# Kernel tuning notes

Measured on AMD Instinct MI355X. Metric: run time of the kernel, lower is better.

Reference implementation:

```python
import jax, jax.numpy as jnp
import numpy as np
import math

NUM_HEADS = 16
SIZE = 1024
HEAD_SIZE = SIZE // NUM_HEADS
B, S = 2, 2048


def setup_inputs() -> dict:
    key = jax.random.key(0)
    ks = jax.random.split(key, 11)
    sc = 1.0 / math.sqrt(SIZE)
    inp = {
        "q": jax.random.normal(ks[0], (B, S, SIZE), dtype=jnp.float32),
        "k": jax.random.normal(ks[1], (B, S, SIZE), dtype=jnp.float32),
        "v": jax.random.normal(ks[2], (B, S, SIZE), dtype=jnp.float32),
        "Wq": jax.random.normal(ks[3], (SIZE, SIZE), dtype=jnp.float32) * sc,
        "bq": jax.random.normal(ks[4], (SIZE,), dtype=jnp.float32) * sc,
        "Wk": jax.random.normal(ks[5], (SIZE, SIZE), dtype=jnp.float32) * sc,
        "bk": jax.random.normal(ks[6], (SIZE,), dtype=jnp.float32) * sc,
        "Wv": jax.random.normal(ks[7], (SIZE, SIZE), dtype=jnp.float32) * sc,
        "bv": jax.random.normal(ks[8], (SIZE,), dtype=jnp.float32) * sc,
        "Wo": jax.random.normal(ks[9], (SIZE, SIZE), dtype=jnp.float32) * sc,
        "bo": jax.random.normal(ks[10], (SIZE,), dtype=jnp.float32) * sc,
    }
    return inp


def _split_heads(x):
    # [B, S, SIZE] -> [B, H, S, D]
    b, s, _ = x.shape
    return x.reshape(b, s, NUM_HEADS, HEAD_SIZE).transpose(0, 2, 1, 3)


def reference(q, k, v, Wq, bq, Wk, bk, Wv, bv, Wo, bo):
    qh = _split_heads(q @ Wq.T + bq) / math.sqrt(HEAD_SIZE)  # [B,H,S,D]
    kh = _split_heads(k @ Wk.T + bk)
    vh = _split_heads(v @ Wv.T + bv)
    scores = jnp.einsum("bhqd,bhkd->bhqk", qh, kh)  # [B,H,S,S]
    attn = jax.nn.softmax(scores, axis=-1)
    ctx = jnp.einsum("bhqk,bhkd->bhqd", attn, vh)  # [B,H,S,D]
    ctx = ctx.transpose(0, 2, 1, 3).reshape(q.shape[0], -1, SIZE)
    return ctx @ Wo.T + bo
```

## Files before the change

kernel.cpp:

```cpp
#include <hip/hip_runtime.h>
#include <hip/hip_bf16.h>

#define SIZE 1024
#define NH 16
#define HD 64
#define BB 2
#define SS 2048
#define MROWS (BB * SS)

using bf16 = __hip_bfloat16;
using frag16 = __attribute__((ext_vector_type(8))) short;
using f32x4 = __attribute__((ext_vector_type(4))) float;
typedef unsigned int u32;

__device__ __forceinline__ void glds16(const bf16* g, bf16* l) {
    __builtin_amdgcn_global_load_lds(
        (const __attribute__((address_space(1))) u32*)g,
        (__attribute__((address_space(3))) u32*)l, 16, 0, 0);
}

__device__ __forceinline__ void cvt_store8(bf16* dst, const float* src) {
    float4 a = *(const float4*)src;
    float4 b = *(const float4*)(src + 4);
    bf16 t[8];
    t[0] = __float2bfloat16(a.x); t[1] = __float2bfloat16(a.y);
    t[2] = __float2bfloat16(a.z); t[3] = __float2bfloat16(a.w);
    t[4] = __float2bfloat16(b.x); t[5] = __float2bfloat16(b.y);
    t[6] = __float2bfloat16(b.z); t[7] = __float2bfloat16(b.w);
    *(uint4*)dst = *(const uint4*)t;
}

__global__ __launch_bounds__(256) void cast_kernel(
    const float* __restrict__ Wq, const float* __restrict__ Wk,
    const float* __restrict__ Wv, const float* __restrict__ Wo,
    const float* __restrict__ q, const float* __restrict__ k,
    const float* __restrict__ v,
    bf16* __restrict__ Wb, bf16* __restrict__ qb,
    bf16* __restrict__ kb, bf16* __restrict__ vb)
{
    const int z = blockIdx.z;
    const float* s; bf16* d; int n;
    switch (z) {
        case 0: s = Wq; d = Wb;                   n = SIZE * SIZE;  break;
        case 1: s = Wk; d = Wb + SIZE * SIZE;     n = SIZE * SIZE;  break;
        case 2: s = Wv; d = Wb + 2 * SIZE * SIZE; n = SIZE * SIZE;  break;
        case 3: s = Wo; d = Wb + 3 * SIZE * SIZE; n = SIZE * SIZE;  break;
        case 4: s = q;  d = qb;                   n = MROWS * SIZE; break;
        case 5: s = k;  d = kb;                   n = MROWS * SIZE; break;
        default: s = v; d = vb;                   n = MROWS * SIZE; break;
    }
    const int i = (blockIdx.x * 256 + threadIdx.x) * 8;
    if (i < n) cvt_store8(d + i, s + i);
}

template <typename YT>
__device__ __forceinline__ void gemm_body(
    const bf16* __restrict__ X, const bf16* __restrict__ W,
    const float* __restrict__ bias, YT* __restrict__ Y, float scale, bool vt_mode)
{
    __shared__ __align__(16) bf16 As[128 * 32];
    __shared__ __align__(16) bf16 Bs[128 * 32];

    const int tid = threadIdx.x;
    const int wave = tid >> 6;
    const int lane = tid & 63;
    const int lane15 = lane & 15;
    const int quad = lane >> 4;
    const int bm = blockIdx.y * 128;
    const int bn = blockIdx.x * 128;
    const int wm = (wave & 1) * 64;
    const int wn = (wave >> 1) * 64;

    f32x4 acc[4][4];
#pragma unroll
    for (int i = 0; i < 4; i++)
#pragma unroll
        for (int j = 0; j < 4; j++)
            acc[i][j] = (f32x4){0.f, 0.f, 0.f, 0.f};

    const int srow = lane >> 2;
    const int scol = (lane & 3) * 8;

    for (int kt = 0; kt < SIZE / 32; kt++) {
        const int k0 = kt * 32;
        __syncthreads();
#pragma unroll
        for (int n = 0; n < 2; n++) {
            const int c = wave * 2 + n;
            glds16(X + (size_t)(bm + c * 16 + srow) * SIZE + k0 + scol, As + c * 512);
            glds16(W + (size_t)(bn + c * 16 + srow) * SIZE + k0 + scol, Bs + c * 512);
        }
        __syncthreads();

        frag16 a[4], b[4];
#pragma unroll
        for (int mi = 0; mi < 4; mi++)
            a[mi] = *(const frag16*)(As + (wm + mi * 16 + lane15) * 32 + quad * 8);
#pragma unroll
        for (int ni = 0; ni < 4; ni++)
            b[ni] = *(const frag16*)(Bs + (wn + ni * 16 + lane15) * 32 + quad * 8);
#pragma unroll
        for (int mi = 0; mi < 4; mi++)
#pragma unroll
            for (int ni = 0; ni < 4; ni++)
                acc[mi][ni] = __builtin_amdgcn_mfma_f32_16x16x32_bf16(
                    a[mi], b[ni], acc[mi][ni], 0, 0, 0);
    }

#pragma unroll
    for (int ni = 0; ni < 4; ni++) {
        const int col = bn + wn + ni * 16 + lane15;
        const float bv = bias[col];
#pragma unroll
        for (int mi = 0; mi < 4; mi++) {
            const int row = bm + wm + mi * 16 + quad * 4;
#pragma unroll
            for (int r = 0; r < 4; r++) {
                float val = (acc[mi][ni][r] + bv) * scale;
                if (vt_mode) {
                    const int rg = row + r;
                    const int bb = rg >> 11, s = rg & (SS - 1);
                    const int hh = col >> 6, d = col & (HD - 1);
                    ((bf16*)Y)[((size_t)(bb * NH + hh) * HD + d) * SS + s] =
                        __float2bfloat16(val);
                } else {
                    Y[(size_t)(row + r) * SIZE + col] = (YT)val;
                }
            }
        }
    }
}

__global__ __launch_bounds__(256) void qkv_proj_kernel(
    const bf16* __restrict__ qb, const bf16* __restrict__ kb, const bf16* __restrict__ vb,
    const bf16* __restrict__ Wb,
    const float* __restrict__ bq, const float* __restrict__ bk, const float* __restrict__ bv,
    bf16* __restrict__ qh, bf16* __restrict__ kh, bf16* __restrict__ vt)
{
    const bf16 *X, *W; const float* bi; bf16* Y; float sc; bool vm;
    if (blockIdx.z == 0)      { X = qb; W = Wb;                   bi = bq; Y = qh; sc = 0.125f; vm = false; }
    else if (blockIdx.z == 1) { X = kb; W = Wb + SIZE * SIZE;     bi = bk; Y = kh; sc = 1.0f;   vm = false; }
    else                      { X = vb; W = Wb + 2 * SIZE * SIZE; bi = bv; Y = vt; sc = 1.0f;   vm = true;  }
    gemm_body<bf16>(X, W, bi, Y, sc, vm);
}

__global__ __launch_bounds__(256) void out_proj_kernel(
    const bf16* __restrict__ ctx, const bf16* __restrict__ Wob,
    const float* __restrict__ bo, float* __restrict__ out)
{
    gemm_body<float>(ctx, Wob, bo, out, 1.0f, false);
}

__global__ __launch_bounds__(256) void attn_kernel(
    const bf16* __restrict__ qh, const bf16* __restrict__ kh,
    const bf16* __restrict__ vt, bf16* __restrict__ ctx)
{
    __shared__ __align__(16) bf16 Ks[64][72];
    __shared__ __align__(16) bf16 Vs[64][72];
    __shared__ __align__(16) bf16 Ps[4][32][72];

    const int tid = threadIdx.x;
    const int wave = tid >> 6;
    const int lane = tid & 63;
    const int lane15 = lane & 15;
    const int quad = lane >> 4;

    const int b = blockIdx.z, h = blockIdx.y;
    const int q0 = blockIdx.x * 128;

    const size_t baseq = (size_t)b * SS * SIZE + (size_t)h * HD;
    const size_t basev = (size_t)(b * NH + h) * HD * SS;
    const float LOG2E = 1.44269504088896340736f;
    const float OFF = 12.0f * LOG2E;

    frag16 aq[2][2];
#pragma unroll
    for (int m = 0; m < 2; m++) {
        const int qrow = q0 + wave * 32 + m * 16 + lane15;
        const bf16* qp = qh + baseq + (size_t)qrow * SIZE + quad * 8;
        aq[m][0] = *(const frag16*)(qp);
        aq[m][1] = *(const frag16*)(qp + 32);
    }

    float l_acc[2][4];
    f32x4 ofrag[2][4];
#pragma unroll
    for (int m = 0; m < 2; m++) {
#pragma unroll
        for (int r = 0; r < 4; r++) l_acc[m][r] = 0.f;
#pragma unroll
        for (int dt = 0; dt < 4; dt++) ofrag[m][dt] = (f32x4){0.f, 0.f, 0.f, 0.f};
    }

    const int sr = tid >> 3;
    const int sc = (tid & 7) * 8;

    for (int kt = 0; kt < SS / 64; kt++) {
        const int s0 = kt * 64;
        __syncthreads();
        *(uint4*)&Ks[sr][sc]      = *(const uint4*)(kh + baseq + (size_t)(s0 + sr) * SIZE + sc);
        *(uint4*)&Ks[sr + 32][sc] = *(const uint4*)(kh + baseq + (size_t)(s0 + sr + 32) * SIZE + sc);
        *(uint4*)&Vs[sr][sc]      = *(const uint4*)(vt + basev + (size_t)sr * SS + s0 + sc);
        *(uint4*)&Vs[sr + 32][sc] = *(const uint4*)(vt + basev + (size_t)(sr + 32) * SS + s0 + sc);
        __syncthreads();

#pragma unroll
        for (int m = 0; m < 2; m++) {
#pragma unroll
            for (int nt = 0; nt < 4; nt++) {
                f32x4 c = (f32x4){0.f, 0.f, 0.f, 0.f};
                c = __builtin_amdgcn_mfma_f32_16x16x32_bf16(
                    aq[m][0], *(const frag16*)&Ks[nt * 16 + lane15][quad * 8], c, 0, 0, 0);
                c = __builtin_amdgcn_mfma_f32_16x16x32_bf16(
                    aq[m][1], *(const frag16*)&Ks[nt * 16 + lane15][32 + quad * 8], c, 0, 0, 0);
#pragma unroll
                for (int r = 0; r < 4; r++) {
                    float p = exp2f(fminf(c[r], 30.f) * LOG2E - OFF);
                    l_acc[m][r] += p;
                    Ps[wave][m * 16 + quad * 4 + r][nt * 16 + lane15] = __float2bfloat16(p);
                }
            }
        }
        __builtin_amdgcn_wave_barrier();

        frag16 ap[2][2];
#pragma unroll
        for (int m = 0; m < 2; m++)
#pragma unroll
            for (int c2 = 0; c2 < 2; c2++)
                ap[m][c2] = *(const frag16*)&Ps[wave][m * 16 + lane15][c2 * 32 + quad * 8];

#pragma unroll
        for (int dt = 0; dt < 4; dt++) {
            frag16 bv0 = *(const frag16*)&Vs[dt * 16 + lane15][quad * 8];
            frag16 bv1 = *(const frag16*)&Vs[dt * 16 + lane15][32 + quad * 8];
#pragma unroll
            for (int m = 0; m < 2; m++) {
                ofrag[m][dt] = __builtin_amdgcn_mfma_f32_16x16x32_bf16(ap[m][0], bv0, ofrag[m][dt], 0, 0, 0);
                ofrag[m][dt] = __builtin_amdgcn_mfma_f32_16x16x32_bf16(ap[m][1], bv1, ofrag[m][dt], 0, 0, 0);
            }
        }
    }

#pragma unroll
    for (int m = 0; m < 2; m++)
#pragma unroll
        for (int r = 0; r < 4; r++) {
            float t = l_acc[m][r];
#pragma unroll
            for (int off = 1; off < 16; off <<= 1)
                t += __shfl_xor(t, off, 16);
            l_acc[m][r] = fmaxf(t, 1e-30f);
        }

#pragma unroll
    for (int m = 0; m < 2; m++)
#pragma unroll
        for (int dt = 0; dt < 4; dt++)
#pragma unroll
            for (int r = 0; r < 4; r++) {
                const int row = q0 + wave * 32 + m * 16 + quad * 4 + r;
                float val = ofrag[m][dt][r] / l_acc[m][r];
                ctx[baseq + (size_t)row * SIZE + dt * 16 + lane15] = __float2bfloat16(val);
            }
}

extern "C" void kernel_launch(void* const* d_in, const int* in_sizes, int n_in,
                              void* d_out, int out_size, void* d_ws, size_t ws_size,
                              hipStream_t stream) {
    const float* q  = (const float*)d_in[0];
    const float* k  = (const float*)d_in[1];
    const float* v  = (const float*)d_in[2];
    const float* Wq = (const float*)d_in[3];
    const float* bq = (const float*)d_in[4];
    const float* Wk = (const float*)d_in[5];
    const float* bk = (const float*)d_in[6];
    const float* Wv = (const float*)d_in[7];
    const float* bv = (const float*)d_in[8];
    const float* Wo = (const float*)d_in[9];
    const float* bo = (const float*)d_in[10];
    float* out = (float*)d_out;

    bf16* Wb  = (bf16*)d_ws;
    bf16* qb  = Wb + (size_t)4 * SIZE * SIZE;
    bf16* kb  = qb + (size_t)MROWS * SIZE;
    bf16* vb  = kb + (size_t)MROWS * SIZE;
    bf16* qh  = vb + (size_t)MROWS * SIZE;
    bf16* kh  = qh + (size_t)MROWS * SIZE;
    bf16* vt  = kh + (size_t)MROWS * SIZE;
    bf16* ctx = vt + (size_t)MROWS * SIZE;

    cast_kernel<<<dim3(MROWS * SIZE / 2048, 1, 7), 256, 0, stream>>>(
        Wq, Wk, Wv, Wo, q, k, v, Wb, qb, kb, vb);
    qkv_proj_kernel<<<dim3(SIZE / 128, MROWS / 128, 3), 256, 0, stream>>>(
        qb, kb, vb, Wb, bq, bk, bv, qh, kh, vt);
    attn_kernel<<<dim3(SS / 128, NH, BB), 256, 0, stream>>>(qh, kh, vt, ctx);
    out_proj_kernel<<<dim3(SIZE / 128, MROWS / 128, 1), 256, 0, stream>>>(
        ctx, Wb + (size_t)3 * SIZE * SIZE, bo, out);
}
```

Before: 295.7 us.

## Split attention KV range in two with combine kernel; transpose V via LDS

The attention kernel now splits the key/value sequence into two halves, one block per half. This doubles the grid and gives more parallelism across CUs. Because the softmax uses a fixed offset, each half writes unnormalized bf16 partial outputs plus row sums, and a new combine kernel adds the halves and normalizes them into ctx. Separately, the V-projection epilogue now stages its tile in shared memory so the transposed V is written with coalesced 16-byte stores instead of scattered 2-byte ones. The costs are an extra kernel launch, extra partial-output traffic, and some precision loss from storing the partials in bf16.

```diff
diff --git a/kernel.cpp b/kernel.cpp
--- a/kernel.cpp
+++ b/kernel.cpp
@@ -7,6 +7,8 @@
 #define BB 2
 #define SS 2048
 #define MROWS (BB * SS)
+#define QT 128
+#define NQT (SS / QT)
 
 using bf16 = __hip_bfloat16;
 using frag16 = __attribute__((ext_vector_type(8))) short;
@@ -58,8 +60,9 @@
     const bf16* __restrict__ X, const bf16* __restrict__ W,
     const float* __restrict__ bias, YT* __restrict__ Y, float scale, bool vt_mode)
 {
-    __shared__ __align__(16) bf16 As[128 * 32];
-    __shared__ __align__(16) bf16 Bs[128 * 32];
+    __shared__ __align__(16) bf16 smem[8704];
+    bf16* As = smem;
+    bf16* Bs = smem + 4096;
 
     const int tid = threadIdx.x;
     const int wave = tid >> 6;
@@ -107,26 +110,53 @@
                     a[mi], b[ni], acc[mi][ni], 0, 0, 0);
     }
 
-#pragma unroll
-    for (int ni = 0; ni < 4; ni++) {
-        const int col = bn + wn + ni * 16 + lane15;
-        const float bv = bias[col];
-#pragma unroll
-        for (int mi = 0; mi < 4; mi++) {
-            const int row = bm + wm + mi * 16 + quad * 4;
-#pragma unroll
-            for (int r = 0; r < 4; r++) {
-                float val = (acc[mi][ni][r] + bv) * scale;
-                if (vt_mode) {
-                    const int rg = row + r;
-                    const int bb = rg >> 11, s = rg & (SS - 1);
-                    const int hh = col >> 6, d = col & (HD - 1);
-                    ((bf16*)Y)[((size_t)(bb * NH + hh) * HD + d) * SS + s] =
-                        __float2bfloat16(val);
-                } else {
+    if (!vt_mode) {
+#pragma unroll
+        for (int ni = 0; ni < 4; ni++) {
+            const int col = bn + wn + ni * 16 + lane15;
+            const float bv = bias[col];
+#pragma unroll
+            for (int mi = 0; mi < 4; mi++) {
+                const int row = bm + wm + mi * 16 + quad * 4;
+#pragma unroll
+                for (int r = 0; r < 4; r++) {
+                    float val = (acc[mi][ni][r] + bv) * scale;
                     Y[(size_t)(row + r) * SIZE + col] = (YT)val;
                 }
             }
+        }
+    } else {
+        bf16* tr = smem;
+        const int bloc = bm >> 11;
+        const int s0g = bm & (SS - 1);
+#pragma unroll
+        for (int p = 0; p < 2; p++) {
+            __syncthreads();
+            if ((wave >> 1) == p) {
+#pragma unroll
+                for (int ni = 0; ni < 4; ni++) {
+                    const int colp = ni * 16 + lane15;
+                    const float bv = bias[bn + p * 64 + colp];
+#pragma unroll
+                    for (int mi = 0; mi < 4; mi++) {
+                        const int row = wm + mi * 16 + quad * 4;
+#pragma unroll
+                        for (int r = 0; r < 4; r++)
+                            tr[colp * 136 + row + r] =
+                                __float2bfloat16(acc[mi][ni][r] + bv);
+                    }
+                }
+            }
+            __syncthreads();
+            const int colp = tid >> 2;
+            const int gcol = bn + p * 64 + colp;
+            const int hh = gcol >> 6, dd = gcol & (HD - 1);
+            bf16* dst = (bf16*)Y + ((size_t)(bloc * NH + hh) * HD + dd) * SS
+                        + s0g + (tid & 3) * 32;
+            const bf16* src = tr + colp * 136 + (tid & 3) * 32;
+#pragma unroll
+            for (int j = 0; j < 4; j++)
+                *(uint4*)(dst + j * 8) = *(const uint4*)(src + j * 8);
         }
     }
 }
@@ -153,7 +183,7 @@
 
 __global__ __launch_bounds__(256) void attn_kernel(
     const bf16* __restrict__ qh, const bf16* __restrict__ kh,
-    const bf16* __restrict__ vt, bf16* __restrict__ ctx)
+    const bf16* __restrict__ vt, bf16* __restrict__ po, float* __restrict__ pl)
 {
     __shared__ __align__(16) bf16 Ks[64][72];
     __shared__ __align__(16) bf16 Vs[64][72];
@@ -166,7 +196,9 @@
     const int quad = lane >> 4;
 
     const int b = blockIdx.z, h = blockIdx.y;
-    const int q0 = blockIdx.x * 128;
+    const int qt = blockIdx.x >> 1;
+    const int sh = blockIdx.x & 1;
+    const int q0 = qt * QT;
 
     const size_t baseq = (size_t)b * SS * SIZE + (size_t)h * HD;
     const size_t basev = (size_t)(b * NH + h) * HD * SS;
@@ -195,8 +227,8 @@
     const int sr = tid >> 3;
     const int sc = (tid & 7) * 8;
 
-    for (int kt = 0; kt < SS / 64; kt++) {
-        const int s0 = kt * 64;
+    for (int kt = 0; kt < (SS / 2) / 64; kt++) {
+        const int s0 = sh * (SS / 2) + kt * 64;
         __syncthreads();
         *(uint4*)&Ks[sr][sc]      = *(const uint4*)(kh + baseq + (size_t)(s0 + sr) * SIZE + sc);
         *(uint4*)&Ks[sr + 32][sc] = *(const uint4*)(kh + baseq + (size_t)(s0 + sr + 32) * SIZE + sc);
@@ -242,6 +274,7 @@
         }
     }
 
+    const int pb = ((b * NH + h) * NQT + qt) * 2 + sh;
 #pragma unroll
     for (int m = 0; m < 2; m++)
 #pragma unroll
@@ -250,19 +283,53 @@
 #pragma unroll
             for (int off = 1; off < 16; off <<= 1)
                 t += __shfl_xor(t, off, 16);
-            l_acc[m][r] = fmaxf(t, 1e-30f);
-        }
-
+            l_acc[m][r] = t;
+        }
+    if (lane15 == 0) {
+        float* plp = pl + (size_t)pb * QT;
+#pragma unroll
+        for (int m = 0; m < 2; m++)
+#pragma unroll
+            for (int r = 0; r < 4; r++)
+                plp[wave * 32 + m * 16 + quad * 4 + r] = l_acc[m][r];
+    }
+    bf16* pop = po + (size_t)pb * QT * HD;
 #pragma unroll
     for (int m = 0; m < 2; m++)
 #pragma unroll
         for (int dt = 0; dt < 4; dt++)
 #pragma unroll
-            for (int r = 0; r < 4; r++) {
-                const int row = q0 + wave * 32 + m * 16 + quad * 4 + r;
-                float val = ofrag[m][dt][r] / l_acc[m][r];
-                ctx[baseq + (size_t)row * SIZE + dt * 16 + lane15] = __float2bfloat16(val);
-            }
+            for (int r = 0; r < 4; r++)
+                pop[(size_t)(wave * 32 + m * 16 + quad * 4 + r) * HD + dt * 16 + lane15] =
+                    __float2bfloat16(ofrag[m][dt][r]);
+}
+
+__global__ __launch_bounds__(256) void combine_kernel(
+    const bf16* __restrict__ po, const float* __restrict__ pl, bf16* __restrict__ ctx)
+{
+    const int b = blockIdx.z, h = blockIdx.y, qt = blockIdx.x;
+    const int tile = (b * NH + h) * NQT + qt;
+    const bf16* p0 = po + (size_t)(tile * 2 + 0) * QT * HD;
+    const bf16* p1 = po + (size_t)(tile * 2 + 1) * QT * HD;
+    const int qr = threadIdx.x >> 1;
+    const int dh = (threadIdx.x & 1) * 32;
+    const float l = pl[(size_t)(tile * 2) * QT + qr] + pl[(size_t)(tile * 2 + 1) * QT + qr];
+    const float inv = 1.0f / fmaxf(l, 1e-30f);
+    bf16* dst = ctx + ((size_t)b * SS + qt * QT + qr) * SIZE + h * HD + dh;
+    const bf16* s0p = p0 + qr * HD + dh;
+    const bf16* s1p = p1 + qr * HD + dh;
+#pragma unroll
+    for (int j = 0; j < 32; j += 8) {
+        uint4 u0 = *(const uint4*)(s0p + j);
+        uint4 u1 = *(const uint4*)(s1p + j);
+        const bf16* a = (const bf16*)&u0;
+        const bf16* bt = (const bf16*)&u1;
+        bf16 o[8];
+#pragma unroll
+        for (int e = 0; e < 8; e++)
+            o[e] = __float2bfloat16((__bfloat162float(a[e]) + __bfloat162float(bt[e])) * inv);
+        *(uint4*)(dst + j) = *(const uint4*)o;
+    }
 }
 
 extern "C" void kernel_launch(void* const* d_in, const int* in_sizes, int n_in,
@@ -288,13 +355,16 @@
     bf16* qh  = vb + (size_t)MROWS * SIZE;
     bf16* kh  = qh + (size_t)MROWS * SIZE;
     bf16* vt  = kh + (size_t)MROWS * SIZE;
-    bf16* ctx = vt + (size_t)MROWS * SIZE;
+    bf16* po  = qb;
+    bf16* ctx = vb;
+    float* pl = (float*)Wb;
 
     cast_kernel<<<dim3(MROWS * SIZE / 2048, 1, 7), 256, 0, stream>>>(
         Wq, Wk, Wv, Wo, q, k, v, Wb, qb, kb, vb);
     qkv_proj_kernel<<<dim3(SIZE / 128, MROWS / 128, 3), 256, 0, stream>>>(
         qb, kb, vb, Wb, bq, bk, bv, qh, kh, vt);
-    attn_kernel<<<dim3(SS / 128, NH, BB), 256, 0, stream>>>(qh, kh, vt, ctx);
+    attn_kernel<<<dim3(NQT * 2, NH, BB), 256, 0, stream>>>(qh, kh, vt, po, pl);
+    combine_kernel<<<dim3(NQT, NH, BB), 256, 0, stream>>>(po, pl, ctx);
     out_proj_kernel<<<dim3(SIZE / 128, MROWS / 128, 1), 256, 0, stream>>>(
         ctx, Wb + (size_t)3 * SIZE * SIZE, bo, out);
 }
```

Measured after the change: 272.9 us. 1.08x faster.
